# Kernel optimization log

Hardware: AMD Instinct MI355X
Metric: run time of the kernel (lower is better)

## Reference

```python
import jax, jax.numpy as jnp
import numpy as np

N = 200000   # num_nodes
D = 64       # embedding_dims
B = 4096     # batch of target nodes (batched per-edge processing)
K = 128      # padded in-neighbor count per target
W = 20       # window_size (history deque length)
H = 128      # hidden_size


def setup_inputs() -> dict:
    key = jax.random.key(0)
    ks = jax.random.split(key, 14)
    return {
        "adj_time": jax.random.uniform(ks[0], (N,), jnp.float32),          # last-seen times in [0,1)
        "gc": jax.random.uniform(ks[1], (N,), jnp.float32),                 # per-node centrality scalar (dict_gc)
        "cur_time": jnp.ones((1,), jnp.float32),                            # current event time (>= all stored times)
        "neigh_mask": jnp.ones((B, K), jnp.float32),                        # 1 = valid neighbor slot
        "hist_feat": jax.random.normal(ks[2], (B, W, 2 * D), jnp.float32),  # feature_dict[...]['feature'] deque
        "hist_time": jax.random.uniform(ks[3], (B, W), jnp.float32),        # feature_dict[...]['time'] deque
        "t2v_w": jax.random.normal(ks[4], (D,), jnp.float32),               # Time2Vec('cos') weights
        "t2v_b": jax.random.normal(ks[5], (D,), jnp.float32),
        "node_w": jax.random.normal(ks[6], (D,), jnp.float32),              # linear_node: Linear(1, D)
        "node_b": jax.random.normal(ks[7], (D,), jnp.float32),
        "att_w": jax.random.normal(ks[8], (2 * D,), jnp.float32),           # Attention: score = cat(a,b) @ w + b
        "att_b": jax.random.normal(ks[9], (1,), jnp.float32),
        "weight": jax.random.normal(ks[10], (H, 4 * D), jnp.float32) * 0.05,
        "targets": jax.random.randint(ks[11], (B,), 0, N),
        "neigh_idx": jax.random.randint(ks[12], (B, K), 0, N),
    }


def reference(adj_time, gc, cur_time, neigh_mask, hist_feat, hist_time,
              t2v_w, t2v_b, node_w, node_b, att_w, att_b, weight,
              targets, neigh_idx):
    t = cur_time[0]

    def node_encoding(idx):
        # Time2Vec('cos'): first channel linear, rest cos(w*dt+b)
        dt = jnp.abs(t - adj_time[idx])[..., None]            # [..., 1]
        phase = t2v_w * dt + t2v_b                            # [..., D]
        tv = jnp.concatenate([phase[..., :1], jnp.cos(phase[..., 1:])], axis=-1)
        feat = jax.nn.relu(tv + gc[idx][..., None] * node_w + node_b)
        # F.normalize (L2 over feature dim)
        return feat / jnp.maximum(jnp.linalg.norm(feat, axis=-1, keepdims=True), 1e-12)

    tgt_feat = node_encoding(targets)       # [B, D]
    ngh_feat = node_encoding(neigh_idx)     # [B, K, D]

    # Decayer(2, 'log'): time_score = 1 / (2 * log(e + dt))
    time_score = 1.0 / (2.0 * jnp.log(jnp.e + (t - adj_time[neigh_idx])))   # [B, K]
    # Attention score between target and each neighbor encoding
    att = (tgt_feat @ att_w[:D])[:, None] \
        + jnp.einsum("bkd,d->bk", ngh_feat, att_w[D:]) + att_b[0]           # [B, K]
    score = jax.nn.leaky_relu(time_score + att, 0.01) * neigh_mask          # [B, K]
    neigh_agg = jnp.einsum("bk,bkd->bd", score, ngh_feat)                   # [B, D]

    combined = jnp.concatenate([tgt_feat, neigh_agg], axis=-1)              # [B, 2D]

    # History aggregation with Decayer(2, 'rev'): w = 1 / (2 * (1 + dt))
    hist_w = 1.0 / (2.0 * (1.0 + (t - hist_time)))                          # [B, W]
    hist_agg = jnp.einsum("bw,bwd->bd", hist_w, hist_feat)                  # [B, 2D]

    feat4 = jnp.concatenate([hist_agg, combined], axis=-1)                  # [B, 4D]
    return jax.nn.relu(feat4 @ weight.T)                                    # [B, H]
```

## Files before the change

kernel.cpp:

```cpp
#include <hip/hip_runtime.h>
#include <math.h>

#define NN 200000
#define DD 64
#define BB 4096
#define KK 128
#define WW 20
#define HH 128
#define TPB 512
#define RPB 8

__device__ __forceinline__ float fast_rcp(float x) { return __builtin_amdgcn_rcpf(x); }
__device__ __forceinline__ float fast_rsq(float x) { return __builtin_amdgcn_rsqf(x); }

__global__ __launch_bounds__(512, 4) void fused(
    const float* __restrict__ adj_time, const float* __restrict__ gc,
    const float* __restrict__ cur_time, const float* __restrict__ neigh_mask,
    const float* __restrict__ hist_feat, const float* __restrict__ hist_time,
    const float* __restrict__ t2v_w, const float* __restrict__ t2v_b,
    const float* __restrict__ node_w, const float* __restrict__ node_b,
    const float* __restrict__ att_w, const float* __restrict__ att_b,
    const float* __restrict__ weight,
    const int* __restrict__ targets, const int* __restrict__ neigh_idx,
    float* __restrict__ out)
{
    const int b0   = blockIdx.x * RPB;
    const int tid  = threadIdx.x;
    const int lane = tid & 63;
    const int wv   = tid >> 6;

    __shared__ float2 dtg[RPB * KK];
    __shared__ float  wk[RPB * KK];
    __shared__ float  hws[RPB][WW];
    __shared__ float  stL[RPB];
    __shared__ float  tile[RPB * 256];
    __shared__ float  wl[128 * 33];

    const float t = cur_time[0];

    float ts_r[2], m_r[2];
#pragma unroll
    for (int i = 0; i < 2; ++i) {
        int   slot = tid + i * TPB;
        int   idx  = neigh_idx[b0 * KK + slot];
        m_r[i]     = neigh_mask[b0 * KK + slot];
        float at   = adj_time[idx];
        float g    = gc[idx];
        dtg[slot]  = make_float2(fabsf(t - at), g);
        ts_r[i]    = fast_rcp(2.0f * __logf(2.71828182845904523536f + (t - at)));
    }
    if (tid < RPB * WW) {
        int r = tid / WW, w = tid - r * WW;
        hws[r][w] = fast_rcp(2.0f * (1.0f + (t - hist_time[(b0 + r) * WW + w])));
    }
    {
        int   tg  = targets[b0 + wv];
        float dtT = fabsf(t - adj_time[tg]);
        float gT  = gc[tg];
        float ph  = fmaf(t2v_w[lane], dtT, t2v_b[lane]);
        float tv_ = (lane == 0) ? ph : __cosf(ph);
        float f   = fmaxf(tv_ + fmaf(gT, node_w[lane], node_b[lane]), 0.f);
        float ss  = f * f;
#pragma unroll
        for (int off = 32; off; off >>= 1) ss += __shfl_xor(ss, off, 64);
        float invn = fast_rsq(fmaxf(ss, 1e-24f));
        float tfn  = f * invn;
        float sdt  = tfn * att_w[lane];
#pragma unroll
        for (int off = 32; off; off >>= 1) sdt += __shfl_xor(sdt, off, 64);
        if (lane == 0) stL[wv] = sdt;
        tile[wv * 256 + 128 + lane] = tfn;
    }
    __syncthreads();

    const float ab = att_b[0];
#pragma unroll
    for (int i = 0; i < 2; ++i) {
        int    slot = tid + i * TPB;
        int    r    = slot >> 7;
        float2 dg   = dtg[slot];
        float  s2 = 0.f, sd = 0.f;
#pragma unroll 8
        for (int d = 0; d < 64; ++d) {
            float ph  = fmaf(t2v_w[d], dg.x, t2v_b[d]);
            float cv  = __cosf(ph);
            float tv_ = (d == 0) ? ph : cv;
            float f   = fmaxf(tv_ + fmaf(dg.y, node_w[d], node_b[d]), 0.f);
            s2 = fmaf(f, f, s2);
            sd = fmaf(f, att_w[64 + d], sd);
        }
        float invn = fast_rsq(fmaxf(s2, 1e-24f));
        float sc   = ts_r[i] + stL[r] + sd * invn + ab;
        sc = (sc > 0.f) ? sc : 0.01f * sc;
        wk[slot] = sc * m_r[i] * invn;
    }

#pragma unroll
    for (int i = 0; i < 2; ++i) {
        int col = tid + i * TPB;
        int r = col >> 7, d = col & 127;
        const float* hf = hist_feat + (size_t)(b0 + r) * WW * 128 + d;
        float s = 0.f;
#pragma unroll
        for (int w = 0; w < WW; ++w) s = fmaf(hws[r][w], hf[w * 128], s);
        tile[r * 256 + d] = s;
    }
    __syncthreads();

    {
        float pw = t2v_w[lane], pb = t2v_b[lane];
        float nw = node_w[lane], nb2 = node_b[lane];
        float acc = 0.f;
        const int base = wv * KK;
#pragma unroll 8
        for (int k = 0; k < KK; ++k) {
            float2 dg = dtg[base + k];
            float  w_ = wk[base + k];
            float  ph = fmaf(pw, dg.x, pb);
            float  cv = __cosf(ph);
            float  tv_ = (lane == 0) ? ph : cv;
            float  f  = fmaxf(tv_ + fmaf(dg.y, nw, nb2), 0.f);
            acc = fmaf(w_, f, acc);
        }
        tile[wv * 256 + 192 + lane] = acc;
    }

    const int h = tid & 127;
    const int g = tid >> 7;
    const float* tb = tile + (g * 2) * 256;
    float acc0 = 0.f, acc1 = 0.f;

    for (int c = 0; c < 8; ++c) {
        __syncthreads();
#pragma unroll
        for (int i = 0; i < 8; ++i) {
            int l  = i * TPB + tid;
            int hh = l >> 5, jj = l & 31;
            wl[hh * 33 + jj] = weight[hh * 256 + c * 32 + jj];
        }
        __syncthreads();

#pragma unroll
        for (int jj = 0; jj < 32; jj += 4) {
            float w0 = wl[h * 33 + jj + 0];
            float w1 = wl[h * 33 + jj + 1];
            float w2 = wl[h * 33 + jj + 2];
            float w3 = wl[h * 33 + jj + 3];
            float4 f0 = *(const float4*)(tb + 0 * 256 + c * 32 + jj);
            float4 f1 = *(const float4*)(tb + 1 * 256 + c * 32 + jj);
            acc0 += w0 * f0.x + w1 * f0.y + w2 * f0.z + w3 * f0.w;
            acc1 += w0 * f1.x + w1 * f1.y + w2 * f1.z + w3 * f1.w;
        }
    }

    out[(size_t)(b0 + g * 2 + 0) * 128 + h] = fmaxf(acc0, 0.f);
    out[(size_t)(b0 + g * 2 + 1) * 128 + h] = fmaxf(acc1, 0.f);
}

extern "C" void kernel_launch(void* const* d_in, const int* in_sizes, int n_in,
                              void* d_out, int out_size, void* d_ws, size_t ws_size,
                              hipStream_t stream) {
    const float* adj_time  = (const float*)d_in[0];
    const float* gc        = (const float*)d_in[1];
    const float* cur_time  = (const float*)d_in[2];
    const float* neigh_mask= (const float*)d_in[3];
    const float* hist_feat = (const float*)d_in[4];
    const float* hist_time = (const float*)d_in[5];
    const float* t2v_w     = (const float*)d_in[6];
    const float* t2v_b     = (const float*)d_in[7];
    const float* node_w    = (const float*)d_in[8];
    const float* node_b    = (const float*)d_in[9];
    const float* att_w     = (const float*)d_in[10];
    const float* att_b     = (const float*)d_in[11];
    const float* weight    = (const float*)d_in[12];
    const int*   targets   = (const int*)d_in[13];
    const int*   neigh_idx = (const int*)d_in[14];

    float* out = (float*)d_out;

    fused<<<BB / RPB, TPB, 0, stream>>>(adj_time, gc, cur_time, neigh_mask,
                                        hist_feat, hist_time, t2v_w, t2v_b,
                                        node_w, node_b, att_w, att_b, weight,
                                        targets, neigh_idx, out);
}
```

Measured before the change: 135.0 us.

## Halve rows per block, split neighbor aggregation across wave pairs, use hardware cos

Rows per block drop from 8 to 4, so each thread handles one neighbor slot and launch bounds allow more resident blocks. The neighbor aggregation is split across two waves per row with a shared-memory partial sum. Per-slot weights are packed into a float4 alongside dt and gc. The aggregation loop calls the hardware cos with the phase pre-scaled by 1/(2π), and the history reduction is vectorised to float4. The cost is reloading the weight matrix into shared memory for twice as many blocks and an extra barrier.

```diff
diff --git a/kernel.cpp b/kernel.cpp
--- a/kernel.cpp
+++ b/kernel.cpp
@@ -8,12 +8,14 @@
 #define WW 20
 #define HH 128
 #define TPB 512
-#define RPB 8
+#define RPB 4
+
+#define INV2PI 0.15915494309189535f
 
 __device__ __forceinline__ float fast_rcp(float x) { return __builtin_amdgcn_rcpf(x); }
 __device__ __forceinline__ float fast_rsq(float x) { return __builtin_amdgcn_rsqf(x); }
 
-__global__ __launch_bounds__(512, 4) void fused(
+__global__ __launch_bounds__(512, 8) void fused(
     const float* __restrict__ adj_time, const float* __restrict__ gc,
     const float* __restrict__ cur_time, const float* __restrict__ neigh_mask,
     const float* __restrict__ hist_feat, const float* __restrict__ hist_time,
@@ -29,31 +31,31 @@
     const int lane = tid & 63;
     const int wv   = tid >> 6;
 
-    __shared__ float2 dtg[RPB * KK];
-    __shared__ float  wk[RPB * KK];
+    __shared__ float4 dtg[RPB * KK];
     __shared__ float  hws[RPB][WW];
     __shared__ float  stL[RPB];
+    __shared__ float  p3p[RPB][DD];
     __shared__ float  tile[RPB * 256];
     __shared__ float  wl[128 * 33];
 
     const float t = cur_time[0];
 
-    float ts_r[2], m_r[2];
-#pragma unroll
-    for (int i = 0; i < 2; ++i) {
-        int   slot = tid + i * TPB;
-        int   idx  = neigh_idx[b0 * KK + slot];
-        m_r[i]     = neigh_mask[b0 * KK + slot];
-        float at   = adj_time[idx];
-        float g    = gc[idx];
-        dtg[slot]  = make_float2(fabsf(t - at), g);
-        ts_r[i]    = fast_rcp(2.0f * __logf(2.71828182845904523536f + (t - at)));
-    }
-    if (tid < RPB * WW) {
-        int r = tid / WW, w = tid - r * WW;
+    const int   slot = tid;
+    const int   idx  = neigh_idx[b0 * KK + slot];
+    const float m    = neigh_mask[b0 * KK + slot];
+    const float at   = adj_time[idx];
+    const float g    = gc[idx];
+    const float dt   = fabsf(t - at);
+    const float ts   = fast_rcp(2.0f * __logf(2.71828182845904523536f + (t - at)));
+    dtg[slot] = make_float4(dt, g, 0.f, 0.f);
+
+    if (tid >= 256 && tid < 256 + RPB * WW) {
+        int i = tid - 256;
+        int r = i / WW, w = i - r * WW;
         hws[r][w] = fast_rcp(2.0f * (1.0f + (t - hist_time[(b0 + r) * WW + w])));
     }
-    {
+
+    if (wv < RPB) {
         int   tg  = targets[b0 + wv];
         float dtT = fabsf(t - adj_time[tg]);
         float gT  = gc[tg];
@@ -73,62 +75,75 @@
     }
     __syncthreads();
 
-    const float ab = att_b[0];
-#pragma unroll
-    for (int i = 0; i < 2; ++i) {
-        int    slot = tid + i * TPB;
-        int    r    = slot >> 7;
-        float2 dg   = dtg[slot];
-        float  s2 = 0.f, sd = 0.f;
-#pragma unroll 8
-        for (int d = 0; d < 64; ++d) {
-            float ph  = fmaf(t2v_w[d], dg.x, t2v_b[d]);
-            float cv  = __cosf(ph);
-            float tv_ = (d == 0) ? ph : cv;
-            float f   = fmaxf(tv_ + fmaf(dg.y, node_w[d], node_b[d]), 0.f);
+    {
+        const int   r  = slot >> 7;
+        const float ab = att_b[0];
+        float s2, sd;
+        {
+            float ph = fmaf(t2v_w[0], dt, t2v_b[0]);
+            float f  = fmaxf(ph + fmaf(g, node_w[0], node_b[0]), 0.f);
+            s2 = f * f;
+            sd = f * att_w[64];
+        }
+#pragma unroll 4
+        for (int d = 1; d < 64; ++d) {
+            float ph = fmaf(t2v_w[d], dt, t2v_b[d]);
+            float f  = fmaxf(__cosf(ph) + fmaf(g, node_w[d], node_b[d]), 0.f);
             s2 = fmaf(f, f, s2);
             sd = fmaf(f, att_w[64 + d], sd);
         }
         float invn = fast_rsq(fmaxf(s2, 1e-24f));
-        float sc   = ts_r[i] + stL[r] + sd * invn + ab;
+        float sc   = ts + stL[r] + sd * invn + ab;
         sc = (sc > 0.f) ? sc : 0.01f * sc;
-        wk[slot] = sc * m_r[i] * invn;
+        dtg[slot].z = sc * m * invn;
     }
 
-#pragma unroll
-    for (int i = 0; i < 2; ++i) {
-        int col = tid + i * TPB;
-        int r = col >> 7, d = col & 127;
-        const float* hf = hist_feat + (size_t)(b0 + r) * WW * 128 + d;
-        float s = 0.f;
-#pragma unroll
-        for (int w = 0; w < WW; ++w) s = fmaf(hws[r][w], hf[w * 128], s);
-        tile[r * 256 + d] = s;
+    if (tid < 128) {
+        int r  = tid >> 5;
+        int c4 = tid & 31;
+        const float4* hf = (const float4*)(hist_feat + (size_t)(b0 + r) * WW * 128) + c4;
+        float4 s4 = make_float4(0.f, 0.f, 0.f, 0.f);
+#pragma unroll 4
+        for (int w = 0; w < WW; ++w) {
+            float  hw = hws[r][w];
+            float4 v  = hf[w * 32];
+            s4.x = fmaf(hw, v.x, s4.x);
+            s4.y = fmaf(hw, v.y, s4.y);
+            s4.z = fmaf(hw, v.z, s4.z);
+            s4.w = fmaf(hw, v.w, s4.w);
+        }
+        *(float4*)(tile + r * 256 + c4 * 4) = s4;
     }
     __syncthreads();
 
+    const int r3   = wv >> 1;
+    const int half = wv & 1;
+    float acc3 = 0.f;
     {
-        float pw = t2v_w[lane], pb = t2v_b[lane];
-        float nw = node_w[lane], nb2 = node_b[lane];
-        float acc = 0.f;
-        const int base = wv * KK;
-#pragma unroll 8
-        for (int k = 0; k < KK; ++k) {
-            float2 dg = dtg[base + k];
-            float  w_ = wk[base + k];
-            float  ph = fmaf(pw, dg.x, pb);
-            float  cv = __cosf(ph);
-            float  tv_ = (lane == 0) ? ph : cv;
-            float  f  = fmaxf(tv_ + fmaf(dg.y, nw, nb2), 0.f);
-            acc = fmaf(w_, f, acc);
+        float sc  = (lane == 0) ? 1.f : INV2PI;
+        float pw  = t2v_w[lane] * sc;
+        float pb  = t2v_b[lane] * sc;
+        float nw  = node_w[lane];
+        float nb2 = node_b[lane];
+        const int base = r3 * KK + half * 64;
+#pragma unroll 4
+        for (int k = 0; k < 64; ++k) {
+            float4 dgw = dtg[base + k];
+            float  ph  = fmaf(pw, dgw.x, pb);
+            float  cv  = __builtin_amdgcn_cosf(ph);
+            float  tv_ = lane ? cv : ph;
+            float  f   = fmaxf(tv_ + fmaf(dgw.y, nw, nb2), 0.f);
+            acc3 = fmaf(dgw.z, f, acc3);
         }
-        tile[wv * 256 + 192 + lane] = acc;
     }
+    if (half) p3p[r3][lane] = acc3;
+    __syncthreads();
+    if (!half) tile[r3 * 256 + 192 + lane] = acc3 + p3p[r3][lane];
 
-    const int h = tid & 127;
-    const int g = tid >> 7;
-    const float* tb = tile + (g * 2) * 256;
-    float acc0 = 0.f, acc1 = 0.f;
+    const int h  = tid & 127;
+    const int gg = tid >> 7;
+    const float* tb = tile + gg * 256;
+    float acc = 0.f;
 
     for (int c = 0; c < 8; ++c) {
         __syncthreads();
@@ -146,15 +161,12 @@
             float w1 = wl[h * 33 + jj + 1];
             float w2 = wl[h * 33 + jj + 2];
             float w3 = wl[h * 33 + jj + 3];
-            float4 f0 = *(const float4*)(tb + 0 * 256 + c * 32 + jj);
-            float4 f1 = *(const float4*)(tb + 1 * 256 + c * 32 + jj);
-            acc0 += w0 * f0.x + w1 * f0.y + w2 * f0.z + w3 * f0.w;
-            acc1 += w0 * f1.x + w1 * f1.y + w2 * f1.z + w3 * f1.w;
+            float4 f0 = *(const float4*)(tb + c * 32 + jj);
+            acc += w0 * f0.x + w1 * f0.y + w2 * f0.z + w3 * f0.w;
         }
     }
 
-    out[(size_t)(b0 + g * 2 + 0) * 128 + h] = fmaxf(acc0, 0.f);
-    out[(size_t)(b0 + g * 2 + 1) * 128 + h] = fmaxf(acc1, 0.f);
+    out[(size_t)(b0 + gg) * 128 + h] = fmaxf(acc, 0.f);
 }
 
 extern "C" void kernel_launch(void* const* d_in, const int* in_sizes, int n_in,
```

Result: slower. 138.2 us (+2.4%).
